# Kernel optimization log

Measured on AMD Instinct MI355X. Metric: run time of the kernel, lower is better.

## Reference

```python
import jax, jax.numpy as jnp
import numpy as np

MAXV = 127.0  # 2**(8-1) - 1, signed int8


def setup_inputs() -> dict:
    key = jax.random.key(0)
    k1, k2, k3 = jax.random.split(key, 3)
    N, K, M = 8192, 4096, 4096  # tokens, size_in, size_out
    x = jax.random.normal(k1, (N, K), dtype=jnp.float32)
    weight = jax.random.normal(k2, (M, K), dtype=jnp.float32) * 0.02
    bias = jax.random.normal(k3, (M,), dtype=jnp.float32) * 0.01
    amax_x = jnp.array([3.0], dtype=jnp.float32)   # calibrated activation amax
    amax_w = jnp.array([0.06], dtype=jnp.float32)  # calibrated weight amax
    return {"x": x, "weight": weight, "bias": bias, "amax_x": amax_x, "amax_w": amax_w}


def _quantize_int8(v, amax):
    # TensorQuantizer with fake_quant=False: scale to int grid, round, clamp to [-127, 127]
    return jnp.clip(jnp.round(v * (MAXV / amax)), -MAXV, MAXV).astype(jnp.int8)


def reference(x, weight, bias, amax_x, amax_w):
    qx = _quantize_int8(x, amax_x)          # [N, K] int8
    qw = _quantize_int8(weight, amax_w)     # [M, K] int8
    acc = jnp.matmul(qx.astype(jnp.int32), qw.T.astype(jnp.int32))  # [N, M] int32
    scale = (MAXV / amax_x) * (MAXV / amax_w)  # combined dequant scale
    out = acc.astype(jnp.float32) / scale
    return out + bias
```

## Files before the change

### kernel.cpp

```cpp
#include <hip/hip_runtime.h>

typedef __attribute__((ext_vector_type(4))) int i32x4;

__device__ __forceinline__ void gload_lds16(const void* g, void* l) {
  __builtin_amdgcn_global_load_lds((const __attribute__((address_space(1))) void*)g,
                                   (__attribute__((address_space(3))) void*)l,
                                   16, 0, 0);
}

#define BARRIER() __builtin_amdgcn_s_barrier()
#define LGKM0()   asm volatile("s_waitcnt lgkmcnt(0)" ::: "memory")
#define VMCNT4()  asm volatile("s_waitcnt vmcnt(4)" ::: "memory")

__global__ void quant_i8_kernel(const float* __restrict__ in,
                                signed char* __restrict__ out,
                                const float* __restrict__ amax, int n4) {
  const float s = 127.0f / amax[0];
  int i = blockIdx.x * blockDim.x + threadIdx.x;
  const int stride = gridDim.x * blockDim.x;
  const float4* __restrict__ in4 = (const float4*)in;
  int* __restrict__ o4 = (int*)out;
  for (; i < n4; i += stride) {
    float4 v = in4[i];
    int q0 = (int)rintf(fminf(fmaxf(v.x * s, -127.0f), 127.0f));
    int q1 = (int)rintf(fminf(fmaxf(v.y * s, -127.0f), 127.0f));
    int q2 = (int)rintf(fminf(fmaxf(v.z * s, -127.0f), 127.0f));
    int q3 = (int)rintf(fminf(fmaxf(v.w * s, -127.0f), 127.0f));
    o4[i] = (q0 & 255) | ((q1 & 255) << 8) | ((q2 & 255) << 16) | ((q3 & 255) << 24);
  }
}

__global__ __launch_bounds__(512, 2) void gemm_i8_8p(
    const signed char* __restrict__ qx,
    const signed char* __restrict__ qw,
    const float* __restrict__ bias,
    const float* __restrict__ amax_x,
    const float* __restrict__ amax_w,
    float* __restrict__ out,
    int N, int M, int K) {
  constexpr int BKB = 128;

  __shared__ signed char lds[4][256 * 128];

  const int tid  = threadIdx.x;
  const int lane = tid & 63;
  const int wid  = tid >> 6;
  const int wm   = wid >> 2;
  const int wn   = wid & 3;
  const int l15  = lane & 15;
  const int l4   = lane >> 4;

  const int nbn = M >> 8;
  const int nwg = (N >> 8) * nbn;
  const int cpx = nwg >> 3;
  const int swz = (blockIdx.x & 7) * cpx + (blockIdx.x >> 3);
  const int rowBase = (swz / nbn) << 8;
  const int colBase = (swz % nbn) << 8;

  const signed char* sA[2][2];
  const signed char* sB[2][2];
#pragma unroll
  for (int h = 0; h < 2; ++h)
#pragma unroll
    for (int L = 0; L < 2; ++L) {
      const int slot = h * 1024 + L * 512 + tid;
      const int row  = slot >> 3;
      const int c    = (slot & 7) ^ (row & 7);
      sA[h][L] = qx + (size_t)(rowBase + row) * K + c * 16;
      sB[h][L] = qw + (size_t)(colBase + row) * K + c * 16;
    }

  signed char* A0 = lds[0];
  signed char* B0 = lds[1];
  signed char* A1 = lds[2];
  signed char* B1 = lds[3];

#define STAGE(dst, src, h, kt)                                             \
  do {                                                                     \
    gload_lds16(src[h][0] + (kt) * BKB, (dst) + (h)*16384 + tid * 16);     \
    gload_lds16(src[h][1] + (kt) * BKB, (dst) + (h)*16384 + 8192 + tid * 16); \
  } while (0)

  const int ck0 = ((l4) ^ (l15 & 7)) * 16;
  const int ck1 = ((4 + l4) ^ (l15 & 7)) * 16;
  const int aRow0 = (wm * 128 + l15) * 128;
  const int bRow0 = (wn * 64 + l15) * 128;

  i32x4 acc[8][4] = {{{0}}};
  i32x4 af[4][2];
  i32x4 bf[4][2];

#define RDA(R, mb)                                                          \
  {                                                                         \
    _Pragma("unroll") for (int mi = 0; mi < 4; ++mi) {                      \
      af[mi][0] = *(const i32x4*)((R) + aRow0 + ((mb) + mi) * 2048 + ck0);  \
      af[mi][1] = *(const i32x4*)((R) + aRow0 + ((mb) + mi) * 2048 + ck1);  \
    }                                                                       \
  }
#define RDB(R, nb)                                                          \
  {                                                                         \
    _Pragma("unroll") for (int nj = 0; nj < 2; ++nj) {                      \
      bf[(nb) + nj][0] = *(const i32x4*)((R) + bRow0 + ((nb) + nj) * 2048 + ck0); \
      bf[(nb) + nj][1] = *(const i32x4*)((R) + bRow0 + ((nb) + nj) * 2048 + ck1); \
    }                                                                       \
  }
#define MFMAQ(mb, nb)                                                       \
  {                                                                         \
    _Pragma("unroll") for (int mi = 0; mi < 4; ++mi)                        \
        _Pragma("unroll") for (int nj = 0; nj < 2; ++nj)                    \
            _Pragma("unroll") for (int ks = 0; ks < 2; ++ks)                \
                acc[(mb) + mi][(nb) + nj] = __builtin_amdgcn_mfma_i32_16x16x64_i8( \
                    af[mi][ks], bf[(nb) + nj][ks], acc[(mb) + mi][(nb) + nj], 0, 0, 0); \
  }

  const int T = K / BKB;

  STAGE(B0, sB, 0, 0); STAGE(B0, sB, 1, 0);
  STAGE(A0, sA, 0, 0); STAGE(A0, sA, 1, 0);
  STAGE(B1, sB, 0, 1); STAGE(B1, sB, 1, 1);
  VMCNT4();
  BARRIER();

  for (int it = 0; it < T / 2; ++it) {
    const int k1 = 2 * it + 1;
    const int k2 = (2 * it + 2 < T) ? 2 * it + 2 : T - 1;
    const int k3 = (2 * it + 3 < T) ? 2 * it + 3 : T - 1;

    RDA(A0, 0); RDB(B0, 0);
    STAGE(A1, sA, 0, k1);
    BARRIER(); LGKM0();
    __builtin_amdgcn_s_setprio(1); MFMAQ(0, 0); __builtin_amdgcn_s_setprio(0);
    BARRIER();

    RDB(B0, 2);
    STAGE(A1, sA, 1, k1);
    BARRIER(); LGKM0();
    __builtin_amdgcn_s_setprio(1); MFMAQ(0, 2); __builtin_amdgcn_s_setprio(0);
    BARRIER();

    RDA(A0, 4);
    STAGE(B0, sB, 0, k2);
    BARRIER(); LGKM0();
    __builtin_amdgcn_s_setprio(1); MFMAQ(4, 0); __builtin_amdgcn_s_setprio(0);
    BARRIER();

    STAGE(B0, sB, 1, k2);
    BARRIER(); LGKM0();
    __builtin_amdgcn_s_setprio(1); MFMAQ(4, 2); __builtin_amdgcn_s_setprio(0);
    VMCNT4();
    BARRIER();

    RDA(A1, 0); RDB(B1, 0);
    STAGE(A0, sA, 0, k2);
    BARRIER(); LGKM0();
    __builtin_amdgcn_s_setprio(1); MFMAQ(0, 0); __builtin_amdgcn_s_setprio(0);
    BARRIER();

    RDB(B1, 2);
    STAGE(A0, sA, 1, k2);
    BARRIER(); LGKM0();
    __builtin_amdgcn_s_setprio(1); MFMAQ(0, 2); __builtin_amdgcn_s_setprio(0);
    BARRIER();

    RDA(A1, 4);
    STAGE(B1, sB, 0, k3);
    BARRIER(); LGKM0();
    __builtin_amdgcn_s_setprio(1); MFMAQ(4, 0); __builtin_amdgcn_s_setprio(0);
    BARRIER();

    STAGE(B1, sB, 1, k3);
    BARRIER(); LGKM0();
    __builtin_amdgcn_s_setprio(1); MFMAQ(4, 2); __builtin_amdgcn_s_setprio(0);
    VMCNT4();
    BARRIER();
  }

  const float dq = amax_x[0] * amax_w[0] * (1.0f / (127.0f * 127.0f));
#pragma unroll
  for (int nj = 0; nj < 4; ++nj) {
    const int col = colBase + wn * 64 + nj * 16 + l15;
    const float bv = bias[col];
#pragma unroll
    for (int mi = 0; mi < 8; ++mi) {
      const int row = rowBase + wm * 128 + mi * 16 + l4 * 4;
#pragma unroll
      for (int r = 0; r < 4; ++r)
        out[(size_t)(row + r) * M + col] = (float)acc[mi][nj][r] * dq + bv;
    }
  }
#undef STAGE
#undef RDA
#undef RDB
#undef MFMAQ
}

extern "C" void kernel_launch(void* const* d_in, const int* in_sizes, int n_in,
                              void* d_out, int out_size, void* d_ws, size_t ws_size,
                              hipStream_t stream) {
  const float* x      = (const float*)d_in[0];
  const float* w      = (const float*)d_in[1];
  const float* bias   = (const float*)d_in[2];
  const float* amax_x = (const float*)d_in[3];
  const float* amax_w = (const float*)d_in[4];
  float* out = (float*)d_out;

  const int M = in_sizes[2];
  const int K = in_sizes[1] / M;
  const int N = (int)((long)in_sizes[0] / K);

  signed char* qx = (signed char*)d_ws;
  signed char* qw = qx + (size_t)N * K;

  quant_i8_kernel<<<2048, 256, 0, stream>>>(x, qx, amax_x, N * (K / 4));
  quant_i8_kernel<<<2048, 256, 0, stream>>>(w, qw, amax_w, M * (K / 4));

  const int nwg = (N / 256) * (M / 256);
  gemm_i8_8p<<<nwg, 512, 0, stream>>>(qx, qw, bias, amax_x, amax_w, out,
                                      N, M, K);
}
```

Before: 191.8 us.

## Shrink GEMM block tile to 128x128 with a 4-phase pipeline and higher occupancy

Changes the int8 GEMM workgroup tile from 256x256 to 128x128, so LDS per block drops to 64KB and register use falls (acc 4x2 instead of 8x4). Launch bounds are raised to 4 blocks per CU, and the ping-pong pipeline is restructured into four phases with vmcnt(2). The intent is more resident waves and more workgroups to hide latency and balance load. In exchange, global-memory reuse per tile is lower, so each block does more loads per MFMA, and barriers per FLOP increase.

```diff
diff --git a/kernel.cpp b/kernel.cpp
--- a/kernel.cpp
+++ b/kernel.cpp
@@ -10,7 +10,7 @@
 
 #define BARRIER() __builtin_amdgcn_s_barrier()
 #define LGKM0()   asm volatile("s_waitcnt lgkmcnt(0)" ::: "memory")
-#define VMCNT4()  asm volatile("s_waitcnt vmcnt(4)" ::: "memory")
+#define VMCNT2()  asm volatile("s_waitcnt vmcnt(2)" ::: "memory")
 
 __global__ void quant_i8_kernel(const float* __restrict__ in,
                                 signed char* __restrict__ out,
@@ -30,7 +30,7 @@
   }
 }
 
-__global__ __launch_bounds__(512, 2) void gemm_i8_8p(
+__global__ __launch_bounds__(512, 4) void gemm_i8_4p(
     const signed char* __restrict__ qx,
     const signed char* __restrict__ qw,
     const float* __restrict__ bias,
@@ -40,7 +40,7 @@
     int N, int M, int K) {
   constexpr int BKB = 128;
 
-  __shared__ signed char lds[4][256 * 128];
+  __shared__ signed char lds[4][128 * 128];
 
   const int tid  = threadIdx.x;
   const int lane = tid & 63;
@@ -50,75 +50,73 @@
   const int l15  = lane & 15;
   const int l4   = lane >> 4;
 
-  const int nbn = M >> 8;
-  const int nwg = (N >> 8) * nbn;
+  const int nbn = M >> 7;
+  const int nwg = (N >> 7) * nbn;
   const int cpx = nwg >> 3;
   const int swz = (blockIdx.x & 7) * cpx + (blockIdx.x >> 3);
-  const int rowBase = (swz / nbn) << 8;
-  const int colBase = (swz % nbn) << 8;
+  const int rowBase = (swz / nbn) << 7;
+  const int colBase = (swz % nbn) << 7;
 
-  const signed char* sA[2][2];
-  const signed char* sB[2][2];
+  const signed char* sA[2];
+  const signed char* sB[2];
 #pragma unroll
-  for (int h = 0; h < 2; ++h)
-#pragma unroll
-    for (int L = 0; L < 2; ++L) {
-      const int slot = h * 1024 + L * 512 + tid;
-      const int row  = slot >> 3;
-      const int c    = (slot & 7) ^ (row & 7);
-      sA[h][L] = qx + (size_t)(rowBase + row) * K + c * 16;
-      sB[h][L] = qw + (size_t)(colBase + row) * K + c * 16;
-    }
+  for (int L = 0; L < 2; ++L) {
+    const int slot = L * 512 + tid;
+    const int row  = slot >> 3;
+    const int c    = (slot & 7) ^ (row & 7);
+    sA[L] = qx + (size_t)(rowBase + row) * K + c * 16;
+    sB[L] = qw + (size_t)(colBase + row) * K + c * 16;
+  }
 
   signed char* A0 = lds[0];
   signed char* B0 = lds[1];
   signed char* A1 = lds[2];
   signed char* B1 = lds[3];
 
-#define STAGE(dst, src, h, kt)                                             \
-  do {                                                                     \
-    gload_lds16(src[h][0] + (kt) * BKB, (dst) + (h)*16384 + tid * 16);     \
-    gload_lds16(src[h][1] + (kt) * BKB, (dst) + (h)*16384 + 8192 + tid * 16); \
+#define STAGE(dst, src, kt)                                  \
+  do {                                                       \
+    gload_lds16(src[0] + (kt) * BKB, (dst) + tid * 16);      \
+    gload_lds16(src[1] + (kt) * BKB, (dst) + 8192 + tid * 16); \
   } while (0)
 
   const int ck0 = ((l4) ^ (l15 & 7)) * 16;
   const int ck1 = ((4 + l4) ^ (l15 & 7)) * 16;
-  const int aRow0 = (wm * 128 + l15) * 128;
-  const int bRow0 = (wn * 64 + l15) * 128;
+  const int aRow0 = (wm * 64 + l15) * 128;
+  const int bRow0 = (wn * 32 + l15) * 128;
 
-  i32x4 acc[8][4] = {{{0}}};
+  i32x4 acc[4][2] = {{{0}}};
   i32x4 af[4][2];
-  i32x4 bf[4][2];
+  i32x4 bf[2][2];
 
 #define RDA(R, mb)                                                          \
   {                                                                         \
-    _Pragma("unroll") for (int mi = 0; mi < 4; ++mi) {                      \
-      af[mi][0] = *(const i32x4*)((R) + aRow0 + ((mb) + mi) * 2048 + ck0);  \
-      af[mi][1] = *(const i32x4*)((R) + aRow0 + ((mb) + mi) * 2048 + ck1);  \
+    _Pragma("unroll") for (int mi = 0; mi < 2; ++mi) {                      \
+      af[(mb) + mi][0] = *(const i32x4*)((R) + aRow0 + ((mb) + mi) * 2048 + ck0); \
+      af[(mb) + mi][1] = *(const i32x4*)((R) + aRow0 + ((mb) + mi) * 2048 + ck1); \
     }                                                                       \
   }
-#define RDB(R, nb)                                                          \
+#define RDB(R)                                                              \
   {                                                                         \
     _Pragma("unroll") for (int nj = 0; nj < 2; ++nj) {                      \
-      bf[(nb) + nj][0] = *(const i32x4*)((R) + bRow0 + ((nb) + nj) * 2048 + ck0); \
-      bf[(nb) + nj][1] = *(const i32x4*)((R) + bRow0 + ((nb) + nj) * 2048 + ck1); \
+      bf[nj][0] = *(const i32x4*)((R) + bRow0 + nj * 2048 + ck0);           \
+      bf[nj][1] = *(const i32x4*)((R) + bRow0 + nj * 2048 + ck1);           \
     }                                                                       \
   }
-#define MFMAQ(mb, nb)                                                       \
+#define MFMAH(mb)                                                           \
   {                                                                         \
-    _Pragma("unroll") for (int mi = 0; mi < 4; ++mi)                        \
+    _Pragma("unroll") for (int mi = 0; mi < 2; ++mi)                        \
         _Pragma("unroll") for (int nj = 0; nj < 2; ++nj)                    \
             _Pragma("unroll") for (int ks = 0; ks < 2; ++ks)                \
-                acc[(mb) + mi][(nb) + nj] = __builtin_amdgcn_mfma_i32_16x16x64_i8( \
-                    af[mi][ks], bf[(nb) + nj][ks], acc[(mb) + mi][(nb) + nj], 0, 0, 0); \
+                acc[(mb) + mi][nj] = __builtin_amdgcn_mfma_i32_16x16x64_i8( \
+                    af[(mb) + mi][ks], bf[nj][ks], acc[(mb) + mi][nj], 0, 0, 0); \
   }
 
   const int T = K / BKB;
 
-  STAGE(B0, sB, 0, 0); STAGE(B0, sB, 1, 0);
-  STAGE(A0, sA, 0, 0); STAGE(A0, sA, 1, 0);
-  STAGE(B1, sB, 0, 1); STAGE(B1, sB, 1, 1);
-  VMCNT4();
+  STAGE(A0, sA, 0);
+  STAGE(B0, sB, 0);
+  STAGE(B1, sB, 1);
+  VMCNT2();
   BARRIER();
 
   for (int it = 0; it < T / 2; ++it) {
@@ -126,63 +124,41 @@
     const int k2 = (2 * it + 2 < T) ? 2 * it + 2 : T - 1;
     const int k3 = (2 * it + 3 < T) ? 2 * it + 3 : T - 1;
 
-    RDA(A0, 0); RDB(B0, 0);
-    STAGE(A1, sA, 0, k1);
+    RDA(A0, 0); RDB(B0);
+    STAGE(A1, sA, k1);
     BARRIER(); LGKM0();
-    __builtin_amdgcn_s_setprio(1); MFMAQ(0, 0); __builtin_amdgcn_s_setprio(0);
+    __builtin_amdgcn_s_setprio(1); MFMAH(0); __builtin_amdgcn_s_setprio(0);
     BARRIER();
 
-    RDB(B0, 2);
-    STAGE(A1, sA, 1, k1);
+    RDA(A0, 2);
+    STAGE(B0, sB, k2);
     BARRIER(); LGKM0();
-    __builtin_amdgcn_s_setprio(1); MFMAQ(0, 2); __builtin_amdgcn_s_setprio(0);
+    __builtin_amdgcn_s_setprio(1); MFMAH(2); __builtin_amdgcn_s_setprio(0);
+    VMCNT2();
     BARRIER();
 
-    RDA(A0, 4);
-    STAGE(B0, sB, 0, k2);
+    RDA(A1, 0); RDB(B1);
+    STAGE(A0, sA, k2);
     BARRIER(); LGKM0();
-    __builtin_amdgcn_s_setprio(1); MFMAQ(4, 0); __builtin_amdgcn_s_setprio(0);
+    __builtin_amdgcn_s_setprio(1); MFMAH(0); __builtin_amdgcn_s_setprio(0);
     BARRIER();
 
-    STAGE(B0, sB, 1, k2);
+    RDA(A1, 2);
+    STAGE(B1, sB, k3);
     BARRIER(); LGKM0();
-    __builtin_amdgcn_s_setprio(1); MFMAQ(4, 2); __builtin_amdgcn_s_setprio(0);
-    VMCNT4();
-    BARRIER();
-
-    RDA(A1, 0); RDB(B1, 0);
-    STAGE(A0, sA, 0, k2);
-    BARRIER(); LGKM0();
-    __builtin_amdgcn_s_setprio(1); MFMAQ(0, 0); __builtin_amdgcn_s_setprio(0);
-    BARRIER();
-
-    RDB(B1, 2);
-    STAGE(A0, sA, 1, k2);
-    BARRIER(); LGKM0();
-    __builtin_amdgcn_s_setprio(1); MFMAQ(0, 2); __builtin_amdgcn_s_setprio(0);
-    BARRIER();
-
-    RDA(A1, 4);
-    STAGE(B1, sB, 0, k3);
-    BARRIER(); LGKM0();
-    __builtin_amdgcn_s_setprio(1); MFMAQ(4, 0); __builtin_amdgcn_s_setprio(0);
-    BARRIER();
-
-    STAGE(B1, sB, 1, k3);
-    BARRIER(); LGKM0();
-    __builtin_amdgcn_s_setprio(1); MFMAQ(4, 2); __builtin_amdgcn_s_setprio(0);
-    VMCNT4();
+    __builtin_amdgcn_s_setprio(1); MFMAH(2); __builtin_amdgcn_s_setprio(0);
+    VMCNT2();
     BARRIER();
   }
 
   const float dq = amax_x[0] * amax_w[0] * (1.0f / (127.0f * 127.0f));
 #pragma unroll
-  for (int nj = 0; nj < 4; ++nj) {
-    const int col = colBase + wn * 64 + nj * 16 + l15;
+  for (int nj = 0; nj < 2; ++nj) {
+    const int col = colBase + wn * 32 + nj * 16 + l15;
     const float bv = bias[col];
 #pragma unroll
-    for (int mi = 0; mi < 8; ++mi) {
-      const int row = rowBase + wm * 128 + mi * 16 + l4 * 4;
+    for (int mi = 0; mi < 4; ++mi) {
+      const int row = rowBase + wm * 64 + mi * 16 + l4 * 4;
 #pragma unroll
       for (int r = 0; r < 4; ++r)
         out[(size_t)(row + r) * M + col] = (float)acc[mi][nj][r] * dq + bv;
@@ -191,7 +167,7 @@
 #undef STAGE
 #undef RDA
 #undef RDB
-#undef MFMAQ
+#undef MFMAH
 }
 
 extern "C" void kernel_launch(void* const* d_in, const int* in_sizes, int n_in,
@@ -214,7 +190,7 @@
   quant_i8_kernel<<<2048, 256, 0, stream>>>(x, qx, amax_x, N * (K / 4));
   quant_i8_kernel<<<2048, 256, 0, stream>>>(w, qw, amax_w, M * (K / 4));
 
-  const int nwg = (N / 256) * (M / 256);
-  gemm_i8_8p<<<nwg, 512, 0, stream>>>(qx, qw, bias, amax_x, amax_w, out,
+  const int nwg = (N / 128) * (M / 128);
+  gemm_i8_4p<<<nwg, 512, 0, stream>>>(qx, qw, bias, amax_x, amax_w, out,
                                       N, M, K);
 }
```

Result: slower. 230.6 us (+20.2%).

## Double-buffer LDS fragment registers and fuse both quantize kernels into one launch

Applied to the files above, without the earlier changes.

The GEMM main loop now holds separate A and B fragment register sets, so all B fragments and the second A half are read from LDS earlier. The explicit lgkmcnt(0) waits are dropped and replaced by sched_barrier fences, with the compiler left to insert the waits needed for correctness. This is meant to overlap LDS reads with MFMA work, at the cost of more VGPRs under launch_bounds(512,2). Separately, the two quantize launches are merged into one kernel that covers x and w, removing one launch and its tail.

```diff
diff --git a/kernel.cpp b/kernel.cpp
--- a/kernel.cpp
+++ b/kernel.cpp
@@ -9,24 +9,33 @@
 }
 
 #define BARRIER() __builtin_amdgcn_s_barrier()
-#define LGKM0()   asm volatile("s_waitcnt lgkmcnt(0)" ::: "memory")
 #define VMCNT4()  asm volatile("s_waitcnt vmcnt(4)" ::: "memory")
-
-__global__ void quant_i8_kernel(const float* __restrict__ in,
-                                signed char* __restrict__ out,
-                                const float* __restrict__ amax, int n4) {
-  const float s = 127.0f / amax[0];
+#define SCHED0()  __builtin_amdgcn_sched_barrier(0)
+
+__global__ void quant_both_kernel(const float* __restrict__ x,
+                                  const float* __restrict__ w,
+                                  signed char* __restrict__ qx,
+                                  signed char* __restrict__ qw,
+                                  const float* __restrict__ amax_x,
+                                  const float* __restrict__ amax_w,
+                                  int nx4, int nw4) {
+  const float sx = 127.0f / amax_x[0];
+  const float sw = 127.0f / amax_w[0];
   int i = blockIdx.x * blockDim.x + threadIdx.x;
   const int stride = gridDim.x * blockDim.x;
-  const float4* __restrict__ in4 = (const float4*)in;
-  int* __restrict__ o4 = (int*)out;
-  for (; i < n4; i += stride) {
-    float4 v = in4[i];
+  const int ntot = nx4 + nw4;
+  for (; i < ntot; i += stride) {
+    const bool isx = i < nx4;
+    const float4* src = isx ? (const float4*)x : (const float4*)w;
+    int* dst = isx ? (int*)qx : (int*)qw;
+    const int j = isx ? i : i - nx4;
+    const float s = isx ? sx : sw;
+    float4 v = src[j];
     int q0 = (int)rintf(fminf(fmaxf(v.x * s, -127.0f), 127.0f));
     int q1 = (int)rintf(fminf(fmaxf(v.y * s, -127.0f), 127.0f));
     int q2 = (int)rintf(fminf(fmaxf(v.z * s, -127.0f), 127.0f));
     int q3 = (int)rintf(fminf(fmaxf(v.w * s, -127.0f), 127.0f));
-    o4[i] = (q0 & 255) | ((q1 & 255) << 8) | ((q2 & 255) << 16) | ((q3 & 255) << 24);
+    dst[j] = (q0 & 255) | ((q1 & 255) << 8) | ((q2 & 255) << 16) | ((q3 & 255) << 24);
   }
 }
 
@@ -87,30 +96,32 @@
   const int bRow0 = (wn * 64 + l15) * 128;
 
   i32x4 acc[8][4] = {{{0}}};
-  i32x4 af[4][2];
-  i32x4 bf[4][2];
-
-#define RDA(R, mb)                                                          \
+  i32x4 afA[4][2], afB[4][2];
+  i32x4 bfA[2][2], bfB[2][2];
+
+#define RD_A(DST, R, mb)                                                    \
   {                                                                         \
     _Pragma("unroll") for (int mi = 0; mi < 4; ++mi) {                      \
-      af[mi][0] = *(const i32x4*)((R) + aRow0 + ((mb) + mi) * 2048 + ck0);  \
-      af[mi][1] = *(const i32x4*)((R) + aRow0 + ((mb) + mi) * 2048 + ck1);  \
+      DST[mi][0] = *(const i32x4*)((R) + aRow0 + ((mb) + mi) * 2048 + ck0); \
+      DST[mi][1] = *(const i32x4*)((R) + aRow0 + ((mb) + mi) * 2048 + ck1); \
     }                                                                       \
   }
-#define RDB(R, nb)                                                          \
+#define RD_B(DST, R, nb)                                                    \
   {                                                                         \
     _Pragma("unroll") for (int nj = 0; nj < 2; ++nj) {                      \
-      bf[(nb) + nj][0] = *(const i32x4*)((R) + bRow0 + ((nb) + nj) * 2048 + ck0); \
-      bf[(nb) + nj][1] = *(const i32x4*)((R) + bRow0 + ((nb) + nj) * 2048 + ck1); \
+      DST[nj][0] = *(const i32x4*)((R) + bRow0 + ((nb) + nj) * 2048 + ck0); \
+      DST[nj][1] = *(const i32x4*)((R) + bRow0 + ((nb) + nj) * 2048 + ck1); \
     }                                                                       \
   }
-#define MFMAQ(mb, nb)                                                       \
+#define MFMAQ(mb, nb, AF, BF)                                               \
   {                                                                         \
+    __builtin_amdgcn_s_setprio(1);                                          \
     _Pragma("unroll") for (int mi = 0; mi < 4; ++mi)                        \
         _Pragma("unroll") for (int nj = 0; nj < 2; ++nj)                    \
             _Pragma("unroll") for (int ks = 0; ks < 2; ++ks)                \
                 acc[(mb) + mi][(nb) + nj] = __builtin_amdgcn_mfma_i32_16x16x64_i8( \
-                    af[mi][ks], bf[(nb) + nj][ks], acc[(mb) + mi][(nb) + nj], 0, 0, 0); \
+                    AF[mi][ks], BF[nj][ks], acc[(mb) + mi][(nb) + nj], 0, 0, 0);   \
+    __builtin_amdgcn_s_setprio(0);                                          \
   }
 
   const int T = K / BKB;
@@ -126,51 +137,53 @@
     const int k2 = (2 * it + 2 < T) ? 2 * it + 2 : T - 1;
     const int k3 = (2 * it + 3 < T) ? 2 * it + 3 : T - 1;
 
-    RDA(A0, 0); RDB(B0, 0);
+    RD_A(afA, A0, 0); RD_B(bfA, B0, 0); RD_B(bfB, B0, 2);
     STAGE(A1, sA, 0, k1);
-    BARRIER(); LGKM0();
-    __builtin_amdgcn_s_setprio(1); MFMAQ(0, 0); __builtin_amdgcn_s_setprio(0);
-    BARRIER();
-
-    RDB(B0, 2);
+    SCHED0();
+    BARRIER();
+    MFMAQ(0, 0, afA, bfA);
+    BARRIER();
+
+    RD_A(afB, A0, 4);
     STAGE(A1, sA, 1, k1);
-    BARRIER(); LGKM0();
-    __builtin_amdgcn_s_setprio(1); MFMAQ(0, 2); __builtin_amdgcn_s_setprio(0);
-    BARRIER();
-
-    RDA(A0, 4);
+    SCHED0();
+    BARRIER();
+    MFMAQ(0, 2, afA, bfB);
+    BARRIER();
+
     STAGE(B0, sB, 0, k2);
-    BARRIER(); LGKM0();
-    __builtin_amdgcn_s_setprio(1); MFMAQ(4, 0); __builtin_amdgcn_s_setprio(0);
+    BARRIER();
+    MFMAQ(4, 0, afB, bfA);
     BARRIER();
 
     STAGE(B0, sB, 1, k2);
-    BARRIER(); LGKM0();
-    __builtin_amdgcn_s_setprio(1); MFMAQ(4, 2); __builtin_amdgcn_s_setprio(0);
+    BARRIER();
+    MFMAQ(4, 2, afB, bfB);
     VMCNT4();
     BARRIER();
 
-    RDA(A1, 0); RDB(B1, 0);
+    RD_A(afA, A1, 0); RD_B(bfA, B1, 0); RD_B(bfB, B1, 2);
     STAGE(A0, sA, 0, k2);
-    BARRIER(); LGKM0();
-    __builtin_amdgcn_s_setprio(1); MFMAQ(0, 0); __builtin_amdgcn_s_setprio(0);
-    BARRIER();
-
-    RDB(B1, 2);
+    SCHED0();
+    BARRIER();
+    MFMAQ(0, 0, afA, bfA);
+    BARRIER();
+
+    RD_A(afB, A1, 4);
     STAGE(A0, sA, 1, k2);
-    BARRIER(); LGKM0();
-    __builtin_amdgcn_s_setprio(1); MFMAQ(0, 2); __builtin_amdgcn_s_setprio(0);
-    BARRIER();
-
-    RDA(A1, 4);
+    SCHED0();
+    BARRIER();
+    MFMAQ(0, 2, afA, bfB);
+    BARRIER();
+
     STAGE(B1, sB, 0, k3);
-    BARRIER(); LGKM0();
-    __builtin_amdgcn_s_setprio(1); MFMAQ(4, 0); __builtin_amdgcn_s_setprio(0);
+    BARRIER();
+    MFMAQ(4, 0, afB, bfA);
     BARRIER();
 
     STAGE(B1, sB, 1, k3);
-    BARRIER(); LGKM0();
-    __builtin_amdgcn_s_setprio(1); MFMAQ(4, 2); __builtin_amdgcn_s_setprio(0);
+    BARRIER();
+    MFMAQ(4, 2, afB, bfB);
     VMCNT4();
     BARRIER();
   }
@@ -189,8 +202,8 @@
     }
   }
 #undef STAGE
-#undef RDA
-#undef RDB
+#undef RD_A
+#undef RD_B
 #undef MFMAQ
 }
 
@@ -211,8 +224,10 @@
   signed char* qx = (signed char*)d_ws;
   signed char* qw = qx + (size_t)N * K;
 
-  quant_i8_kernel<<<2048, 256, 0, stream>>>(x, qx, amax_x, N * (K / 4));
-  quant_i8_kernel<<<2048, 256, 0, stream>>>(w, qw, amax_w, M * (K / 4));
+  const int nx4 = N * (K / 4);
+  const int nw4 = M * (K / 4);
+  quant_both_kernel<<<2048, 256, 0, stream>>>(x, w, qx, qw, amax_x, amax_w,
+                                              nx4, nw4);
 
   const int nwg = (N / 256) * (M / 256);
   gemm_i8_8p<<<nwg, 512, 0, stream>>>(qx, qw, bias, amax_x, amax_w, out,
```

Result: no change. 191.9 us (+0.0%).
